# Kernel tuning notes

Hardware: AMD Instinct MI355X
Metric: run time of the kernel (lower is better)

Reference implementation:

```python
import jax, jax.numpy as jnp
import numpy as np

B, C, HW, P = 8, 128, 50176, 128  # batch, channels, flattened spatial, num parcels

def setup_inputs() -> dict:
    key = jax.random.key(0)
    k1, k2 = jax.random.split(key)
    x = jax.random.normal(k1, (B, C, HW), dtype=jnp.float32)
    # 0/1 parcel assignment mask [b, num_parcs, hw]
    parcel_mask_batch = jax.random.randint(k2, (B, P, HW), 0, 2).astype(jnp.float32)
    return {"x": x, "parcel_mask_batch": parcel_mask_batch}

def reference(x, parcel_mask_batch):
    # torch: for each i, x[i] @ mask[i].T  -> stacked [b, c, num_parcs]
    # out[b, c, p] = sum_hw x[b, c, hw] * mask[b, p, hw]
    return jnp.einsum('bch,bph->bcp', x, parcel_mask_batch)
```

## Files before the change

kernel.cpp:

```cpp
#include <hip/hip_runtime.h>
#include <hip/hip_bf16.h>

typedef float f32x4 __attribute__((ext_vector_type(4)));
typedef short short8 __attribute__((ext_vector_type(8)));

#define BATCH 8
#define CH    128
#define HWN   50176
#define PN    128
#define KSPLIT 64
#define KWIN  784
#define BK    32
#define NFULL 24
#define TAILOFF (NFULL*BK)

__device__ __forceinline__ ushort f2bf_rn(float f){
  uint u = __float_as_uint(f);
  u += 0x7FFFu + ((u >> 16) & 1u);
  return (ushort)(u >> 16);
}
__device__ __forceinline__ float bf2f(ushort h){
  return __uint_as_float(((uint)h) << 16);
}

__device__ __forceinline__ short8 cvt8_trunc(f32x4 a, f32x4 b){
  union{ short8 v; ushort u[8]; } r;
  r.u[0]=(ushort)(__float_as_uint(a.x)>>16); r.u[1]=(ushort)(__float_as_uint(a.y)>>16);
  r.u[2]=(ushort)(__float_as_uint(a.z)>>16); r.u[3]=(ushort)(__float_as_uint(a.w)>>16);
  r.u[4]=(ushort)(__float_as_uint(b.x)>>16); r.u[5]=(ushort)(__float_as_uint(b.y)>>16);
  r.u[6]=(ushort)(__float_as_uint(b.z)>>16); r.u[7]=(ushort)(__float_as_uint(b.w)>>16);
  return r.v;
}

__device__ __forceinline__ void cvt8_hilo(f32x4 a, f32x4 b, short8& h8, short8& l8){
  union{ short8 v; ushort u[8]; } h, l;
  float f[8] = {a.x,a.y,a.z,a.w,b.x,b.y,b.z,b.w};
  #pragma unroll
  for(int j=0;j<8;++j){
    ushort hh = f2bf_rn(f[j]);
    h.u[j] = hh;
    l.u[j] = f2bf_rn(f[j] - bf2f(hh));
  }
  h8 = h.v; l8 = l.v;
}

__device__ __forceinline__ void gload16(const float* g, float* l){
  __builtin_amdgcn_global_load_lds(
      (const __attribute__((address_space(1))) void*)g,
      (__attribute__((address_space(3))) void*)l, 16, 0, 0);
}

__device__ __forceinline__ f32x4 lds_read4(const float* base, int r, int slot){
  return *(const f32x4*)(base + r*32 + ((slot ^ (r&7)) << 2));
}
__device__ __forceinline__ void lds_write4(float* base, int r, int slot, f32x4 v){
  *(f32x4*)(base + r*32 + ((slot ^ (r&7)) << 2)) = v;
}

template<int EPI>
__global__ __launch_bounds__(256, 2)
void raggr_kernel(const float* __restrict__ X, const float* __restrict__ Mk,
                  float* __restrict__ OUT, float* __restrict__ PART){
  __shared__ float lds[2][2][4096];

  const int tid  = threadIdx.x;
  const int b    = blockIdx.x >> 6;
  const int s    = blockIdx.x & 63;
  const int lane = tid & 63;
  const int w    = tid >> 6;
  const int wrow = (w >> 1) * 64;
  const int wcol = (w & 1) * 64;

  const size_t base = (size_t)b * CH * HWN + (size_t)s * KWIN;
  const f32x4 z4 = {0.f,0.f,0.f,0.f};

  f32x4 acc[4][4];
  #pragma unroll
  for(int m=0;m<4;++m)
    #pragma unroll
    for(int n=0;n<4;++n) acc[m][n] = z4;

  const int lrow = lane >> 3;
  const int kq   = (lane & 7) ^ lrow;
  const float* pX[4]; const float* pM[4];
  #pragma unroll
  for(int i=0;i<4;++i){
    int r = w*32 + i*8 + lrow;
    pX[i] = X  + base + (size_t)r * HWN + kq*4;
    pM[i] = Mk + base + (size_t)r * HWN + kq*4;
  }

  #define STAGE(tt, buf) {                                                    \
    _Pragma("unroll")                                                         \
    for(int i=0;i<4;++i){                                                     \
      gload16(pX[i] + (tt)*BK, &lds[buf][0][(w*4+i)*256]);                    \
      gload16(pM[i] + (tt)*BK, &lds[buf][1][(w*4+i)*256]);                    \
    } }

  #define COMPUTE(buf) {                                                      \
    const float* Xb = lds[buf][0];                                            \
    const float* Mb = lds[buf][1];                                            \
    const int l15 = lane & 15;                                                \
    const int s0  = (lane >> 4) * 2;                                          \
    short8 bf[4], ah[4], al[4];                                               \
    _Pragma("unroll")                                                         \
    for(int n=0;n<4;++n){                                                     \
      int r = wcol + n*16 + l15;                                              \
      bf[n] = cvt8_trunc(lds_read4(Mb, r, s0), lds_read4(Mb, r, s0+1));       \
    }                                                                         \
    _Pragma("unroll")                                                         \
    for(int m=0;m<4;++m){                                                     \
      int r = wrow + m*16 + l15;                                              \
      cvt8_hilo(lds_read4(Xb, r, s0), lds_read4(Xb, r, s0+1), ah[m], al[m]);  \
    }                                                                         \
    _Pragma("unroll")                                                         \
    for(int m=0;m<4;++m)                                                      \
      _Pragma("unroll")                                                       \
      for(int n=0;n<4;++n){                                                   \
        acc[m][n] = __builtin_amdgcn_mfma_f32_16x16x32_bf16(ah[m], bf[n], acc[m][n], 0,0,0); \
        acc[m][n] = __builtin_amdgcn_mfma_f32_16x16x32_bf16(al[m], bf[n], acc[m][n], 0,0,0); \
      }                                                                       \
  }

  STAGE(0, 0);
  __syncthreads();

  #pragma unroll 1
  for(int t=0; t<NFULL; ++t){
    if(t+1 < NFULL) STAGE(t+1, (t+1)&1);
    COMPUTE(t&1);
    __syncthreads();
  }

  {
    int r    = tid >> 1;
    int half = tid & 1;
    size_t g = base + (size_t)r * HWN + TAILOFF + half*8;
    f32x4 x0 = *(const f32x4*)(X + g),  x1 = *(const f32x4*)(X + g + 4);
    f32x4 m0 = *(const f32x4*)(Mk + g), m1 = *(const f32x4*)(Mk + g + 4);
    float* Xb = lds[0][0]; float* Mb = lds[0][1];
    lds_write4(Xb, r, half*2,   x0); lds_write4(Xb, r, half*2+1, x1);
    lds_write4(Xb, r, 4+half*2, z4); lds_write4(Xb, r, 5+half*2, z4);
    lds_write4(Mb, r, half*2,   m0); lds_write4(Mb, r, half*2+1, m1);
    lds_write4(Mb, r, 4+half*2, z4); lds_write4(Mb, r, 5+half*2, z4);
    __syncthreads();
    COMPUTE(0);
  }

  if(EPI == 0){
    float* p = PART + ((size_t)(b*KSPLIT + s)) * 16384;
    #pragma unroll
    for(int m=0;m<4;++m){
      int row0 = wrow + m*16 + ((lane >> 4) << 2);
      #pragma unroll
      for(int n=0;n<4;++n){
        int col = wcol + n*16 + (lane & 15);
        #pragma unroll
        for(int j=0;j<4;++j) p[(size_t)(row0+j)*128 + col] = acc[m][n][j];
      }
    }
  } else {
    float* o = OUT + (size_t)b * 16384;
    #pragma unroll
    for(int m=0;m<4;++m){
      int row0 = wrow + m*16 + ((lane >> 4) << 2);
      #pragma unroll
      for(int n=0;n<4;++n){
        int col = wcol + n*16 + (lane & 15);
        #pragma unroll
        for(int j=0;j<4;++j) atomicAdd(&o[(size_t)(row0+j)*128 + col], acc[m][n][j]);
      }
    }
  }
  #undef STAGE
  #undef COMPUTE
}

__global__ void reduce_kernel(const float* __restrict__ PART, float* __restrict__ OUT){
  int idx = blockIdx.x * 256 + threadIdx.x;
  int b   = idx >> 12;
  int c4  = idx & 4095;
  const f32x4* p = (const f32x4*)PART;
  f32x4 sum = {0.f,0.f,0.f,0.f};
  size_t base_ = (size_t)b * KSPLIT * 4096 + (size_t)c4;
  #pragma unroll 8
  for(int s2=0; s2<KSPLIT; ++s2) sum += p[base_ + (size_t)s2*4096];
  ((f32x4*)OUT)[idx] = sum;
}

__global__ void zero_kernel(float* __restrict__ OUT){
  int idx = blockIdx.x * 256 + threadIdx.x;
  if(idx < BATCH*CH*PN) OUT[idx] = 0.f;
}

extern "C" void kernel_launch(void* const* d_in, const int* in_sizes, int n_in,
                              void* d_out, int out_size, void* d_ws, size_t ws_size,
                              hipStream_t stream){
  const float* X  = (const float*)d_in[0];
  const float* Mk = (const float*)d_in[1];
  float* O = (float*)d_out;

  const size_t part_bytes = (size_t)BATCH * KSPLIT * CH * PN * sizeof(float);
  if(ws_size >= part_bytes && d_ws != nullptr){
    float* part = (float*)d_ws;
    raggr_kernel<0><<<dim3(BATCH*KSPLIT), dim3(256), 0, stream>>>(X, Mk, O, part);
    reduce_kernel<<<dim3(128), dim3(256), 0, stream>>>(part, O);
  } else {
    zero_kernel<<<dim3(512), dim3(256), 0, stream>>>(O);
    raggr_kernel<1><<<dim3(BATCH*KSPLIT), dim3(256), 0, stream>>>(X, Mk, O, nullptr);
  }
}
```

Before: 431.5 us.

## Restructure GEMM-reduce into 512-thread blocks with 4-stage async LDS pipeline

Halves the K-split so each block covers a 1568-wide window, which divides evenly into BK chunks and removes the scalar tail path. Blocks grow to 8 waves: half load X and half load the mask, and a 4-buffer ring with explicit vmcnt waits and a raw s_barrier keeps three stages in flight. The split-K partial layout and the reduce kernel are rearranged to match, and the hi part of the X split now truncates instead of rounding. The aim is to hide global-load latency better and cut barrier overhead. The cost is a single block per CU with a larger LDS footprint, and barrier correctness now depends on the hand-written vmcnt counts.

```diff
diff --git a/kernel.cpp b/kernel.cpp
--- a/kernel.cpp
+++ b/kernel.cpp
@@ -8,11 +8,10 @@
 #define CH    128
 #define HWN   50176
 #define PN    128
-#define KSPLIT 64
-#define KWIN  784
+#define KSPLIT 32
+#define KWIN  1568
 #define BK    32
-#define NFULL 24
-#define TAILOFF (NFULL*BK)
+#define NST   49
 
 __device__ __forceinline__ ushort f2bf_rn(float f){
   uint u = __float_as_uint(f);
@@ -37,7 +36,7 @@
   float f[8] = {a.x,a.y,a.z,a.w,b.x,b.y,b.z,b.w};
   #pragma unroll
   for(int j=0;j<8;++j){
-    ushort hh = f2bf_rn(f[j]);
+    ushort hh = (ushort)(__float_as_uint(f[j]) >> 16);
     h.u[j] = hh;
     l.u[j] = f2bf_rn(f[j] - bf2f(hh));
   }
@@ -53,58 +52,57 @@
 __device__ __forceinline__ f32x4 lds_read4(const float* base, int r, int slot){
   return *(const f32x4*)(base + r*32 + ((slot ^ (r&7)) << 2));
 }
-__device__ __forceinline__ void lds_write4(float* base, int r, int slot, f32x4 v){
-  *(f32x4*)(base + r*32 + ((slot ^ (r&7)) << 2)) = v;
-}
 
 template<int EPI>
-__global__ __launch_bounds__(256, 2)
+__global__ __launch_bounds__(512, 1)
 void raggr_kernel(const float* __restrict__ X, const float* __restrict__ Mk,
                   float* __restrict__ OUT, float* __restrict__ PART){
-  __shared__ float lds[2][2][4096];
+  __shared__ float lds[4 * 8192];
 
   const int tid  = threadIdx.x;
-  const int b    = blockIdx.x >> 6;
-  const int s    = blockIdx.x & 63;
+  const int b    = blockIdx.x >> 5;
+  const int s    = blockIdx.x & 31;
   const int lane = tid & 63;
   const int w    = tid >> 6;
-  const int wrow = (w >> 1) * 64;
-  const int wcol = (w & 1) * 64;
+  const int wrow = (w >> 2) * 64;
+  const int wcol = (w & 3) * 32;
 
   const size_t base = (size_t)b * CH * HWN + (size_t)s * KWIN;
   const f32x4 z4 = {0.f,0.f,0.f,0.f};
 
-  f32x4 acc[4][4];
+  f32x4 acc[4][2];
   #pragma unroll
-  for(int m=0;m<4;++m)
-    #pragma unroll
-    for(int n=0;n<4;++n) acc[m][n] = z4;
+  for(int m=0;m<4;++m){ acc[m][0]=z4; acc[m][1]=z4; }
 
   const int lrow = lane >> 3;
   const int kq   = (lane & 7) ^ lrow;
-  const float* pX[4]; const float* pM[4];
+  const float* SRC = (w >= 4) ? Mk : X;
+  const float* ps[4];
+  float* ld0[4];
   #pragma unroll
   for(int i=0;i<4;++i){
-    int r = w*32 + i*8 + lrow;
-    pX[i] = X  + base + (size_t)r * HWN + kq*4;
-    pM[i] = Mk + base + (size_t)r * HWN + kq*4;
+    int r = (w & 3)*32 + i*8 + lrow;
+    ps[i]  = SRC + base + (size_t)r * HWN + kq*4;
+    ld0[i] = lds + ((w >= 4) ? 4096 : 0) + ((w & 3)*32 + i*8)*32;
   }
 
-  #define STAGE(tt, buf) {                                                    \
-    _Pragma("unroll")                                                         \
-    for(int i=0;i<4;++i){                                                     \
-      gload16(pX[i] + (tt)*BK, &lds[buf][0][(w*4+i)*256]);                    \
-      gload16(pM[i] + (tt)*BK, &lds[buf][1][(w*4+i)*256]);                    \
-    } }
+  #define STAGE(tt) {                                                         \
+    float* dst = ld0[0] + ((tt) & 3) * 8192;                                  \
+    const size_t go = (size_t)(tt) * BK;                                      \
+    gload16(ps[0] + go, dst);                                                 \
+    gload16(ps[1] + go, ld0[1] + ((tt) & 3) * 8192);                          \
+    gload16(ps[2] + go, ld0[2] + ((tt) & 3) * 8192);                          \
+    gload16(ps[3] + go, ld0[3] + ((tt) & 3) * 8192);                          \
+  }
 
-  #define COMPUTE(buf) {                                                      \
-    const float* Xb = lds[buf][0];                                            \
-    const float* Mb = lds[buf][1];                                            \
+  #define COMPUTE(tt) {                                                       \
+    const float* Xb = lds + ((tt) & 3) * 8192;                                \
+    const float* Mb = Xb + 4096;                                              \
     const int l15 = lane & 15;                                                \
     const int s0  = (lane >> 4) * 2;                                          \
-    short8 bf[4], ah[4], al[4];                                               \
+    short8 bf[2], ah[4], al[4];                                               \
     _Pragma("unroll")                                                         \
-    for(int n=0;n<4;++n){                                                     \
+    for(int n=0;n<2;++n){                                                     \
       int r = wcol + n*16 + l15;                                              \
       bf[n] = cvt8_trunc(lds_read4(Mb, r, s0), lds_read4(Mb, r, s0+1));       \
     }                                                                         \
@@ -116,47 +114,34 @@
     _Pragma("unroll")                                                         \
     for(int m=0;m<4;++m)                                                      \
       _Pragma("unroll")                                                       \
-      for(int n=0;n<4;++n){                                                   \
+      for(int n=0;n<2;++n){                                                   \
         acc[m][n] = __builtin_amdgcn_mfma_f32_16x16x32_bf16(ah[m], bf[n], acc[m][n], 0,0,0); \
         acc[m][n] = __builtin_amdgcn_mfma_f32_16x16x32_bf16(al[m], bf[n], acc[m][n], 0,0,0); \
       }                                                                       \
   }
 
-  STAGE(0, 0);
-  __syncthreads();
+  STAGE(0); STAGE(1); STAGE(2);
 
   #pragma unroll 1
-  for(int t=0; t<NFULL; ++t){
-    if(t+1 < NFULL) STAGE(t+1, (t+1)&1);
-    COMPUTE(t&1);
-    __syncthreads();
-  }
-
-  {
-    int r    = tid >> 1;
-    int half = tid & 1;
-    size_t g = base + (size_t)r * HWN + TAILOFF + half*8;
-    f32x4 x0 = *(const f32x4*)(X + g),  x1 = *(const f32x4*)(X + g + 4);
-    f32x4 m0 = *(const f32x4*)(Mk + g), m1 = *(const f32x4*)(Mk + g + 4);
-    float* Xb = lds[0][0]; float* Mb = lds[0][1];
-    lds_write4(Xb, r, half*2,   x0); lds_write4(Xb, r, half*2+1, x1);
-    lds_write4(Xb, r, 4+half*2, z4); lds_write4(Xb, r, 5+half*2, z4);
-    lds_write4(Mb, r, half*2,   m0); lds_write4(Mb, r, half*2+1, m1);
-    lds_write4(Mb, r, 4+half*2, z4); lds_write4(Mb, r, 5+half*2, z4);
-    __syncthreads();
-    COMPUTE(0);
+  for(int t=0; t<NST; ++t){
+    if(t < NST-2)       asm volatile("s_waitcnt vmcnt(8)" ::: "memory");
+    else if(t == NST-2) asm volatile("s_waitcnt vmcnt(4)" ::: "memory");
+    else                asm volatile("s_waitcnt vmcnt(0)" ::: "memory");
+    __builtin_amdgcn_s_barrier();
+    if(t+3 < NST) STAGE(t+3);
+    COMPUTE(t);
   }
 
   if(EPI == 0){
-    float* p = PART + ((size_t)(b*KSPLIT + s)) * 16384;
     #pragma unroll
     for(int m=0;m<4;++m){
       int row0 = wrow + m*16 + ((lane >> 4) << 2);
       #pragma unroll
-      for(int n=0;n<4;++n){
+      for(int n=0;n<2;++n){
         int col = wcol + n*16 + (lane & 15);
         #pragma unroll
-        for(int j=0;j<4;++j) p[(size_t)(row0+j)*128 + col] = acc[m][n][j];
+        for(int j=0;j<4;++j)
+          PART[(size_t)b*524288 + (size_t)(row0+j)*4096 + s*128 + col] = acc[m][n][j];
       }
     }
   } else {
@@ -165,7 +150,7 @@
     for(int m=0;m<4;++m){
       int row0 = wrow + m*16 + ((lane >> 4) << 2);
       #pragma unroll
-      for(int n=0;n<4;++n){
+      for(int n=0;n<2;++n){
         int col = wcol + n*16 + (lane & 15);
         #pragma unroll
         for(int j=0;j<4;++j) atomicAdd(&o[(size_t)(row0+j)*128 + col], acc[m][n][j]);
@@ -177,15 +162,15 @@
 }
 
 __global__ void reduce_kernel(const float* __restrict__ PART, float* __restrict__ OUT){
-  int idx = blockIdx.x * 256 + threadIdx.x;
-  int b   = idx >> 12;
-  int c4  = idx & 4095;
-  const f32x4* p = (const f32x4*)PART;
-  f32x4 sum = {0.f,0.f,0.f,0.f};
-  size_t base_ = (size_t)b * KSPLIT * 4096 + (size_t)c4;
+  int bid = blockIdx.x;
+  int b   = bid >> 6;
+  int c   = (bid & 63)*2 + (threadIdx.x >> 7);
+  int p   = threadIdx.x & 127;
+  size_t base_ = (size_t)b*524288 + (size_t)c*4096 + p;
+  float sum = 0.f;
   #pragma unroll 8
-  for(int s2=0; s2<KSPLIT; ++s2) sum += p[base_ + (size_t)s2*4096];
-  ((f32x4*)OUT)[idx] = sum;
+  for(int k=0;k<32;++k) sum += PART[base_ + k*128];
+  OUT[(size_t)b*16384 + c*128 + p] = sum;
 }
 
 __global__ void zero_kernel(float* __restrict__ OUT){
@@ -203,10 +188,10 @@
   const size_t part_bytes = (size_t)BATCH * KSPLIT * CH * PN * sizeof(float);
   if(ws_size >= part_bytes && d_ws != nullptr){
     float* part = (float*)d_ws;
-    raggr_kernel<0><<<dim3(BATCH*KSPLIT), dim3(256), 0, stream>>>(X, Mk, O, part);
-    reduce_kernel<<<dim3(128), dim3(256), 0, stream>>>(part, O);
+    raggr_kernel<0><<<dim3(BATCH*KSPLIT), dim3(512), 0, stream>>>(X, Mk, O, part);
+    reduce_kernel<<<dim3(512), dim3(256), 0, stream>>>(part, O);
   } else {
     zero_kernel<<<dim3(512), dim3(256), 0, stream>>>(O);
-    raggr_kernel<1><<<dim3(BATCH*KSPLIT), dim3(256), 0, stream>>>(X, Mk, O, nullptr);
+    raggr_kernel<1><<<dim3(BATCH*KSPLIT), dim3(512), 0, stream>>>(X, Mk, O, nullptr);
   }
 }
```

New measurement: 421.7 us. 1.02x faster.
